# Kernel optimization log

Hardware: AMD Instinct MI355X
Metric: run time of the kernel (lower is better)

## Reference

```python
import jax, jax.numpy as jnp
import numpy as np

B, S, D, H = 4, 2048, 512, 8


def _ln(x, g, b, eps=1e-5):
    m = x.mean(-1, keepdims=True)
    v = ((x - m) ** 2).mean(-1, keepdims=True)
    return (x - m) / jnp.sqrt(v + eps) * g + b


def setup_inputs() -> dict:
    key = jax.random.key(0)
    ks = iter(jax.random.split(key, 32))
    n = lambda shape, s=0.02: jax.random.normal(next(ks), shape, jnp.float32) * s
    z = lambda *shape: jnp.zeros(shape, jnp.float32)
    o = lambda *shape: jnp.ones(shape, jnp.float32)
    return {
        "x": jax.random.normal(next(ks), (B, S, D), jnp.float32),
        "x_prev": jax.random.normal(next(ks), (B, S, D), jnp.float32),
        "mu": jnp.float32(0.5),
        "in_proj_w": n((3 * D, D)), "in_proj_b": z(3 * D),
        "out_w": n((D, D)), "out_b": z(D),
        "ln1_g": o(D), "ln1_b": z(D),
        "time_mod": jnp.full((D,), 0.5, jnp.float32),
        "sm_ln_g": o(D), "sm_ln_b": z(D),
        "wr_w": n((D, D)), "wr_b": z(D),
        "wv_w": n((D, D)), "wv_b": z(D),
        "sc_ln_g": o(D), "sc_ln_b": z(D),
        "ln2_g": o(D), "ln2_b": z(D),
        "w1": n((4 * D, D)), "b1": z(4 * D),
        "w2": n((D, 4 * D)), "b2": z(D),
        "ln3_g": o(D), "ln3_b": z(D),
    }


def reference(x, x_prev, mu, in_proj_w, in_proj_b, out_w, out_b, ln1_g, ln1_b,
              time_mod, sm_ln_g, sm_ln_b, wr_w, wr_b, wv_w, wv_b,
              sc_ln_g, sc_ln_b, ln2_g, ln2_b, w1, b1, w2, b2, ln3_g, ln3_b):
    Bs, Sl, Dm = x.shape
    hd = Dm // H
    # Shift (x_prev is not None)
    shifted = mu * x + (1.0 - mu) * x_prev
    # Multihead self-attention (eval mode; dropout = identity)
    qkv = shifted @ in_proj_w.T + in_proj_b
    q, k, v = jnp.split(qkv, 3, axis=-1)
    q = q.reshape(Bs, Sl, H, hd)
    k = k.reshape(Bs, Sl, H, hd)
    v = v.reshape(Bs, Sl, H, hd)
    scores = jnp.einsum('bqhd,bkhd->bhqk', q, k) / jnp.sqrt(jnp.float32(hd))
    attn = jax.nn.softmax(scores, axis=-1)
    ao = jnp.einsum('bhqk,bkhd->bqhd', attn, v).reshape(Bs, Sl, Dm)
    ao = ao @ out_w.T + out_b
    x1 = _ln(shifted + ao, ln1_g, ln1_b)
    # SequenceMergingSeq with C = V = W = x1: sequential decayed running sums
    def step(carry, xt):  # xt: [B, D]
        a, b = carry
        decay = jax.nn.sigmoid(xt * time_mod)
        e = jnp.exp(xt)
        a = decay.mean(-1, keepdims=True) * a + e.sum(-1, keepdims=True)
        b = decay * b + e * xt
        return (a, b), b / (a + 1e-8)
    a0 = jnp.zeros((Bs, 1), x1.dtype)
    b0 = jnp.zeros((Bs, Dm), x1.dtype)
    _, outs = jax.lax.scan(step, (a0, b0), jnp.swapaxes(x1, 0, 1))  # [S,B,D]
    merged = _ln(jnp.swapaxes(outs, 0, 1), sm_ln_g, sm_ln_b)
    # StateCoupling
    coupled = _ln(jax.nn.sigmoid(merged @ wr_w.T + wr_b) * (merged @ wv_w.T + wv_b),
                  sc_ln_g, sc_ln_b)
    x2 = _ln(x1 + coupled, ln2_g, ln2_b)
    # FFN
    ffn = jax.nn.relu(x2 @ w1.T + b1) @ w2.T + b2
    return _ln(x2 + ffn, ln3_g, ln3_b)
```

## Files before the change

kernel.cpp:

```cpp
#include <hip/hip_runtime.h>
#include <math.h>

#define D_MODEL 512
#define SEQ     2048
#define BATCH   4
#define NH      8
#define HD      64
#define CHUNK   32
#define NCHUNK  64
#define M_TOK   (BATCH*SEQ)

typedef __attribute__((ext_vector_type(8))) short bhalf8;
typedef __attribute__((ext_vector_type(4))) float f32x4;

__device__ __forceinline__ float sigmoidf_(float x){ return 1.f/(1.f+expf(-x)); }

__device__ __forceinline__ unsigned short f2b(float f){
  unsigned u = __float_as_uint(f);
  u += 0x7FFFu + ((u>>16)&1u);
  return (unsigned short)(u>>16);
}
__device__ __forceinline__ float b2f(unsigned short h){
  return __uint_as_float(((unsigned)h)<<16);
}
__device__ __forceinline__ float blo(unsigned v){ return __uint_as_float(v<<16); }
__device__ __forceinline__ float bhi(unsigned v){ return __uint_as_float(v & 0xFFFF0000u); }
__device__ __forceinline__ unsigned bpack(float a, float b){
  return (unsigned)f2b(a) | ((unsigned)f2b(b)<<16);
}

__device__ __forceinline__ void gll16(const void* g, void* l){
  __builtin_amdgcn_global_load_lds(
      (const __attribute__((address_space(1))) unsigned int*)g,
      (__attribute__((address_space(3))) unsigned int*)l, 16, 0, 0);
}

__device__ __forceinline__ float exp2_hw(float x){
  float r;
  asm volatile("v_exp_f32 %0, %1" : "=v"(r) : "v"(x));
  return r;
}

__device__ __forceinline__ void block_sum2(float& a, float& b, float* lds){
  #pragma unroll
  for (int o=32;o>0;o>>=1){ a += __shfl_xor(a,o); b += __shfl_xor(b,o); }
  int w = threadIdx.x>>6, l = threadIdx.x&63;
  if (l==0){ lds[2*w]=a; lds[2*w+1]=b; }
  __syncthreads();
  float ta=0.f, tb=0.f; int nw = blockDim.x>>6;
  for (int i=0;i<nw;++i){ ta+=lds[2*i]; tb+=lds[2*i+1]; }
  a=ta; b=tb;
  __syncthreads();
}

__global__ void cvtshift_k(const float* __restrict__ s0,const float* __restrict__ s1,
                           const float* __restrict__ s2,const float* __restrict__ s3,
                           const float* __restrict__ s4,const float* __restrict__ s5,
                           unsigned short* __restrict__ d0,unsigned short* __restrict__ d1,
                           unsigned short* __restrict__ d2,unsigned short* __restrict__ d3,
                           unsigned short* __restrict__ d4,unsigned short* __restrict__ d5,
                           const float* __restrict__ x, const float* __restrict__ xp,
                           const float* __restrict__ mu,
                           unsigned short* __restrict__ ob){
  int t = blockIdx.x*blockDim.x + threadIdx.x;
  if (t < 917504){
    int j = t;
    const float* s; unsigned short* d;
    if (j < 196608){ s=s0; d=d0; }
    else if ((j-=196608) < 65536){ s=s1; d=d1; }
    else if ((j-=65536)  < 65536){ s=s2; d=d2; }
    else if ((j-=65536)  < 65536){ s=s3; d=d3; }
    else if ((j-=65536)  < 262144){ s=s4; d=d4; }
    else { j-=262144; s=s5; d=d5; }
    float4 v = ((const float4*)s)[j];
    uint2 p; p.x = bpack(v.x, v.y); p.y = bpack(v.z, v.w);
    ((uint2*)d)[j] = p;
  } else {
    int i = t - 917504;
    float m = mu[0];
    float4 a = ((const float4*)x)[i], p = ((const float4*)xp)[i];
    float4 r;
    r.x = m*a.x + (1.f-m)*p.x; r.y = m*a.y + (1.f-m)*p.y;
    r.z = m*a.z + (1.f-m)*p.z; r.w = m*a.w + (1.f-m)*p.w;
    uint2 q; q.x = bpack(r.x, r.y); q.y = bpack(r.z, r.w);
    ((uint2*)ob)[i] = q;
  }
}

template<int ACT, int OUTB>
__global__ __launch_bounds__(256) void mgemm_k(const unsigned short* __restrict__ A,
    const unsigned short* __restrict__ W, const float* __restrict__ bias,
    float* __restrict__ Yf, unsigned short* __restrict__ Yb, int Nd, int K){
  __shared__ unsigned short As[128*64];
  __shared__ unsigned short Bs[128*64];
  const int tid = threadIdx.x;
  const int w = tid>>6, lane = tid&63;
  const int l15 = lane&15, l4 = lane>>4;
  const int wr = w>>1, wc = w&1;
  const int nwg = gridDim.x*gridDim.y;
  const int orig = blockIdx.y*gridDim.x + blockIdx.x;
  const int swz = (orig&7)*(nwg>>3) + (orig>>3);
  const int bn = swz % gridDim.x;
  const int bm = swz / gridDim.x;

  const size_t Kb = (size_t)K*2;
  const int srow  = lane>>3;
  const int sbyte = ((lane&7)*16) ^ (srow<<4);
  const char* Ag = (const char*)A + (size_t)(bm*128)*Kb + sbyte;
  const char* Wg = (const char*)W + (size_t)(bn*128)*Kb + sbyte;

  f32x4 acc[4][4];
  const f32x4 z = {0.f,0.f,0.f,0.f};
  #pragma unroll
  for (int i=0;i<4;++i)
    #pragma unroll
    for (int j=0;j<4;++j) acc[i][j] = z;

  const int KT = K/64;
  for (int kt=0; kt<KT; ++kt){
    if (kt) __syncthreads();
    const size_t kOff = (size_t)kt*128;
    #pragma unroll
    for (int i=0;i<4;++i){
      int c = w*4 + i;
      int r = c*8 + srow;
      gll16(Ag + (size_t)r*Kb + kOff, (char*)As + c*1024);
      gll16(Wg + (size_t)r*Kb + kOff, (char*)Bs + c*1024);
    }
    __syncthreads();

    bhalf8 af[4][2], bf_[4][2];
    #pragma unroll
    for (int fr=0; fr<4; ++fr){
      int row = wr*64 + fr*16 + l15;
      #pragma unroll
      for (int ks=0; ks<2; ++ks){
        int byo = (l4*16 + ks*64) ^ ((row&7)<<4);
        af[fr][ks] = *(const bhalf8*)((const char*)As + row*128 + byo);
      }
    }
    #pragma unroll
    for (int fc=0; fc<4; ++fc){
      int row = wc*64 + fc*16 + l15;
      #pragma unroll
      for (int ks=0; ks<2; ++ks){
        int byo = (l4*16 + ks*64) ^ ((row&7)<<4);
        bf_[fc][ks] = *(const bhalf8*)((const char*)Bs + row*128 + byo);
      }
    }
    #pragma unroll
    for (int ks=0; ks<2; ++ks)
      #pragma unroll
      for (int fr=0; fr<4; ++fr)
        #pragma unroll
        for (int fc=0; fc<4; ++fc)
          acc[fr][fc] = __builtin_amdgcn_mfma_f32_16x16x32_bf16(af[fr][ks], bf_[fc][ks], acc[fr][fc], 0, 0, 0);
  }

  const int rowBase = bm*128 + wr*64;
  const int colBase = bn*128 + wc*64;
  #pragma unroll
  for (int fc=0; fc<4; ++fc){
    int col = colBase + fc*16 + l15;
    float bv = bias[col];
    #pragma unroll
    for (int fr=0; fr<4; ++fr){
      #pragma unroll
      for (int j=0; j<4; ++j){
        int row = rowBase + fr*16 + l4*4 + j;
        float v = acc[fr][fc][j] + bv;
        if (ACT) v = fmaxf(v, 0.f);
        if (OUTB) Yb[(size_t)row*Nd + col] = f2b(v);
        else      Yf[(size_t)row*Nd + col] = v;
      }
    }
  }
}

template<int ACT, int FUSE2, int SPLITK>
__global__ __launch_bounds__(256) void mgemm64_k(const unsigned short* __restrict__ A,
    const unsigned short* __restrict__ W0, const unsigned short* __restrict__ W1v,
    const float* __restrict__ bias0, const float* __restrict__ bias1,
    unsigned short* __restrict__ Yb0, unsigned short* __restrict__ Yb1,
    int Nd, int K){
  __shared__ unsigned short As[128*64];
  __shared__ unsigned short Bs[64*64];
  const int tid = threadIdx.x;
  const int w = tid>>6, lane = tid&63;
  const int l15 = lane&15, l4 = lane>>4;
  const int wr = w>>1, wc = w&1;
  const int nwg = gridDim.x*gridDim.y;
  const int orig = blockIdx.y*gridDim.x + blockIdx.x;
  const int swz = (orig&7)*(nwg>>3) + (orig>>3);
  int bn = swz % gridDim.x;
  const int bm = swz / gridDim.x;
  const unsigned short* W = W0;
  const float* bias = bias0;
  unsigned short* Yb = Yb0;
  int half = 0;
  if (FUSE2 && bn >= 8){ W = W1v; bias = bias1; Yb = Yb1; bn -= 8; }
  if (SPLITK && bn >= 8){ half = 1; Yb = Yb1; bn -= 8; }

  const int Ksr = SPLITK ? (K>>1) : K;
  const size_t Kb = (size_t)K*2;
  const size_t hOff = (size_t)half * Ksr * 2;
  const int srow  = lane>>3;
  const int sbyte = ((lane&7)*16) ^ (srow<<4);
  const char* Ag = (const char*)A + (size_t)(bm*128)*Kb + hOff + sbyte;
  const char* Wg = (const char*)W + (size_t)(bn*64)*Kb + hOff + sbyte;

  f32x4 acc[4][2];
  const f32x4 z = {0.f,0.f,0.f,0.f};
  #pragma unroll
  for (int i=0;i<4;++i)
    #pragma unroll
    for (int j=0;j<2;++j) acc[i][j] = z;

  const int KT = Ksr/64;
  for (int kt=0; kt<KT; ++kt){
    if (kt) __syncthreads();
    const size_t kOff = (size_t)kt*128;
    #pragma unroll
    for (int i=0;i<4;++i){
      int c = w*4 + i;
      int r = c*8 + srow;
      gll16(Ag + (size_t)r*Kb + kOff, (char*)As + c*1024);
    }
    #pragma unroll
    for (int i=0;i<2;++i){
      int c = w*2 + i;
      int r = c*8 + srow;
      gll16(Wg + (size_t)r*Kb + kOff, (char*)Bs + c*1024);
    }
    __syncthreads();

    bhalf8 af[4][2], bf_[2][2];
    #pragma unroll
    for (int fr=0; fr<4; ++fr){
      int row = wr*64 + fr*16 + l15;
      #pragma unroll
      for (int ks=0; ks<2; ++ks){
        int byo = (l4*16 + ks*64) ^ ((row&7)<<4);
        af[fr][ks] = *(const bhalf8*)((const char*)As + row*128 + byo);
      }
    }
    #pragma unroll
    for (int fc=0; fc<2; ++fc){
      int row = wc*32 + fc*16 + l15;
      #pragma unroll
      for (int ks=0; ks<2; ++ks){
        int byo = (l4*16 + ks*64) ^ ((row&7)<<4);
        bf_[fc][ks] = *(const bhalf8*)((const char*)Bs + row*128 + byo);
      }
    }
    #pragma unroll
    for (int ks=0; ks<2; ++ks)
      #pragma unroll
      for (int fr=0; fr<4; ++fr)
        #pragma unroll
        for (int fc=0; fc<2; ++fc)
          acc[fr][fc] = __builtin_amdgcn_mfma_f32_16x16x32_bf16(af[fr][ks], bf_[fc][ks], acc[fr][fc], 0, 0, 0);
  }

  const int rowBase = bm*128 + wr*64;
  const int colBase = bn*64 + wc*32;
  #pragma unroll
  for (int fc=0; fc<2; ++fc){
    int col = colBase + fc*16 + l15;
    float bv = (SPLITK && half) ? 0.f : bias[col];
    #pragma unroll
    for (int fr=0; fr<4; ++fr){
      #pragma unroll
      for (int j=0; j<4; ++j){
        int row = rowBase + fr*16 + l4*4 + j;
        float v = acc[fr][fc][j] + bv;
        if (ACT) v = fmaxf(v, 0.f);
        Yb[(size_t)row*Nd + col] = f2b(v);
      }
    }
  }
}

__global__ __launch_bounds__(512, 4) void fattn_k(const unsigned short* __restrict__ qkv,
                                                  unsigned short* __restrict__ ao){
  __shared__ unsigned short Ks[2][64*64];
  __shared__ unsigned short Vt[2][64*64];
  __shared__ unsigned short Ps[128*64];
  const int nwg = gridDim.x*gridDim.y*gridDim.z;
  const int orig = (blockIdx.z*gridDim.y + blockIdx.y)*gridDim.x + blockIdx.x;
  const int swz = (orig&7)*(nwg>>3) + (orig>>3);
  const int qt = swz % gridDim.x;
  const int rem = swz / gridDim.x;
  const int h = rem % gridDim.y;
  const int b = rem / gridDim.y;
  const int tid = threadIdx.x, w = tid>>6, lane = tid&63;
  const int l15 = lane&15, l4 = lane>>4;
  const size_t rowB = 3072;
  const char* base = (const char*)qkv + (size_t)b*SEQ*rowB;
  const char* Kg = base + 1024 + h*128;
  const char* Vg = base + 2048 + h*128;
  const float C2 = 0.18033688f;

  bhalf8 qf[2];
  {
    const char* qrow = base + (size_t)(qt*128 + w*16 + l15)*rowB + h*128;
    qf[0] = *(const bhalf8*)(qrow + l4*16);
    qf[1] = *(const bhalf8*)(qrow + l4*16 + 64);
  }
  bhalf8 v1;
  {
    short o = (l15==0) ? (short)0x3F80 : (short)0;
    v1 = (bhalf8){o,o,o,o,o,o,o,o};
  }

  const f32x4 z = {0.f,0.f,0.f,0.f};
  f32x4 oa[4], ol = z;
  #pragma unroll
  for (int i=0;i<4;++i) oa[i] = z;
  float mj = -INFINITY;

  const int srow  = lane>>3;
  const int sbyte = ((lane&7)*16) ^ (srow<<4);
  const int vd = lane;
  const int vsel = (vd>>3)&1;

  unsigned short vload[8];
  {
    int r = w*8 + srow;
    gll16(Kg + (size_t)r*rowB + sbyte, (char*)Ks[0] + w*1024);
  }
  #pragma unroll
  for (int i=0;i<8;++i)
    vload[i] = *(const unsigned short*)(Vg + (size_t)(w*8 + i)*rowB + vd*2);

  int cur = 0;
  for (int kt=0; kt<SEQ/64; ++kt){
    #pragma unroll
    for (int i=0;i<2;++i){
      int p = i ^ vsel;
      unsigned lo = (unsigned)vload[p*4+0] | ((unsigned)vload[p*4+1]<<16);
      unsigned hi = (unsigned)vload[p*4+2] | ((unsigned)vload[p*4+3]<<16);
      uint2 pk; pk.x = lo; pk.y = hi;
      int byo = (w*16 + p*8) ^ ((vd&7)<<4);
      *(uint2*)((char*)Vt[cur] + vd*128 + byo) = pk;
    }
    __syncthreads();

    if (kt+1 < SEQ/64){
      int r = w*8 + srow;
      gll16(Kg + (size_t)((kt+1)*64 + r)*rowB + sbyte, (char*)Ks[cur^1] + w*1024);
      #pragma unroll
      for (int i=0;i<8;++i)
        vload[i] = *(const unsigned short*)(Vg + (size_t)((kt+1)*64 + w*8 + i)*rowB + vd*2);
    }

    bhalf8 kf[4][2];
    #pragma unroll
    for (int fc=0; fc<4; ++fc){
      int kr = fc*16 + l15;
      #pragma unroll
      for (int ks=0; ks<2; ++ks){
        int byo = (l4*16 + ks*64) ^ ((kr&7)<<4);
        kf[fc][ks] = *(const bhalf8*)((const char*)Ks[cur] + kr*128 + byo);
      }
    }
    f32x4 s[4];
    #pragma unroll
    for (int i=0;i<4;++i) s[i] = z;
    __builtin_amdgcn_s_setprio(1);
    #pragma unroll
    for (int ks=0; ks<2; ++ks)
      #pragma unroll
      for (int fc=0; fc<4; ++fc)
        s[fc] = __builtin_amdgcn_mfma_f32_16x16x32_bf16(kf[fc][ks], qf[ks], s[fc], 0, 0, 0);
    __builtin_amdgcn_s_setprio(0);

    {
      float rm0 = fmaxf(fmaxf(s[0][0],s[0][1]), fmaxf(s[0][2],s[0][3]));
      float rm1 = fmaxf(fmaxf(s[1][0],s[1][1]), fmaxf(s[1][2],s[1][3]));
      float rm2 = fmaxf(fmaxf(s[2][0],s[2][1]), fmaxf(s[2][2],s[2][3]));
      float rm3 = fmaxf(fmaxf(s[3][0],s[3][1]), fmaxf(s[3][2],s[3][3]));
      float rm = fmaxf(fmaxf(rm0,rm1), fmaxf(rm2,rm3));
      rm = fmaxf(rm, __shfl_xor(rm,16));
      rm = fmaxf(rm, __shfl_xor(rm,32));
      float tmax = rm * C2;
      if (__any(tmax > mj + 8.f)){
        float mn = fmaxf(mj, tmax);
        float sc = exp2_hw(mj - mn);
        mj = mn;
        float scj0 = __shfl(sc, l4*4+0), scj1 = __shfl(sc, l4*4+1);
        float scj2 = __shfl(sc, l4*4+2), scj3 = __shfl(sc, l4*4+3);
        #pragma unroll
        for (int fc=0; fc<4; ++fc){
          oa[fc][0] *= scj0; oa[fc][1] *= scj1;
          oa[fc][2] *= scj2; oa[fc][3] *= scj3;
        }
        ol[0] *= scj0; ol[1] *= scj1; ol[2] *= scj2; ol[3] *= scj3;
      }
      int qrow = w*16 + l15;
      #pragma unroll
      for (int fc=0; fc<4; ++fc){
        float p0 = exp2_hw(fmaf(C2, s[fc][0], -mj));
        float p1 = exp2_hw(fmaf(C2, s[fc][1], -mj));
        float p2 = exp2_hw(fmaf(C2, s[fc][2], -mj));
        float p3 = exp2_hw(fmaf(C2, s[fc][3], -mj));
        unsigned lo, hi;
        asm volatile("v_cvt_pk_bf16_f32 %0, %1, %2" : "=v"(lo) : "v"(p0), "v"(p1));
        asm volatile("v_cvt_pk_bf16_f32 %0, %1, %2" : "=v"(hi) : "v"(p2), "v"(p3));
        uint2 pk; pk.x = lo; pk.y = hi;
        int byo = (fc*32 + l4*8) ^ ((l15&7)<<4);
        *(uint2*)((char*)Ps + qrow*128 + byo) = pk;
      }
    }

    bhalf8 vf[4][2];
    #pragma unroll
    for (int fc=0; fc<4; ++fc){
      int d = fc*16 + l15;
      #pragma unroll
      for (int ks=0; ks<2; ++ks){
        int byo = (ks*64 + l4*16) ^ ((d&7)<<4);
        vf[fc][ks] = *(const bhalf8*)((const char*)Vt[cur] + d*128 + byo);
      }
    }
    {
      int qrow = w*16 + l15;
      bhalf8 pf[2];
      #pragma unroll
      for (int ks=0; ks<2; ++ks){
        int byo = (ks*64 + l4*16) ^ ((l15&7)<<4);
        pf[ks] = *(const bhalf8*)((const char*)Ps + qrow*128 + byo);
      }
      __builtin_amdgcn_s_setprio(1);
      #pragma unroll
      for (int ks=0; ks<2; ++ks){
        #pragma unroll
        for (int fc=0; fc<4; ++fc)
          oa[fc] = __builtin_amdgcn_mfma_f32_16x16x32_bf16(pf[ks], vf[fc][ks], oa[fc], 0, 0, 0);
        ol = __builtin_amdgcn_mfma_f32_16x16x32_bf16(pf[ks], v1, ol, 0, 0, 0);
      }
      __builtin_amdgcn_s_setprio(0);
    }
    cur ^= 1;
  }

  {
    float li[4];
    #pragma unroll
    for (int j=0;j<4;++j) li[j] = 1.f/__shfl(ol[j], l4<<4);
    #pragma unroll
    for (int fc=0; fc<4; ++fc){
      int col = h*64 + fc*16 + l15;
      size_t r0 = (size_t)(b*SEQ + qt*128 + w*16 + l4*4);
      ao[(r0+0)*D_MODEL + col] = f2b(oa[fc][0]*li[0]);
      ao[(r0+1)*D_MODEL + col] = f2b(oa[fc][1]*li[1]);
      ao[(r0+2)*D_MODEL + col] = f2b(oa[fc][2]*li[2]);
      ao[(r0+3)*D_MODEL + col] = f2b(oa[fc][3]*li[3]);
    }
  }
}

__global__ __launch_bounds__(256) void lnfin_k(const unsigned int* __restrict__ X2b,
    const unsigned int* __restrict__ F0, const unsigned int* __restrict__ F1,
    const float* __restrict__ g, const float* __restrict__ be, float* __restrict__ outf){
  __shared__ float lds[16];
  const size_t off2 = (size_t)blockIdx.x * 256;
  const int tid = threadIdx.x;
  unsigned xv = X2b[off2+tid], f0 = F0[off2+tid], f1 = F1[off2+tid];
  float a0 = blo(xv) + blo(f0) + blo(f1);
  float a1 = bhi(xv) + bhi(f0) + bhi(f1);
  float s1 = a0+a1, s2 = a0*a0+a1*a1;
  block_sum2(s1, s2, lds);
  float mean = s1 * (1.f/512.f);
  float var  = s2 * (1.f/512.f) - mean*mean;
  float rstd = rsqrtf(var + 1e-5f);
  float2 gg = ((const float2*)g)[tid], bb = ((const float2*)be)[tid];
  float2 r;
  r.x = (a0-mean)*rstd*gg.x + bb.x;
  r.y = (a1-mean)*rstd*gg.y + bb.y;
  ((float2*)outf)[off2+tid] = r;
}

__global__ __launch_bounds__(256) void ln_scan_k(const unsigned int* __restrict__ Ab,
    const unsigned int* __restrict__ Pb,
    const float* __restrict__ g, const float* __restrict__ be, const float* __restrict__ tm,
    unsigned int* __restrict__ x1b, unsigned int* __restrict__ dec, unsigned int* __restrict__ u,
    float* __restrict__ dm, float* __restrict__ es){
  __shared__ float lds[16];
  const size_t row = blockIdx.x;
  const size_t off2 = row * 256;
  const int tid = threadIdx.x;
  unsigned av = Ab[off2+tid], pv = Pb[off2+tid];
  float a0 = blo(av) + blo(pv);
  float a1 = bhi(av) + bhi(pv);
  float s1 = a0+a1, s2 = a0*a0+a1*a1;
  block_sum2(s1, s2, lds);
  float mean = s1 * (1.f/512.f);
  float var  = s2 * (1.f/512.f) - mean*mean;
  float rstd = rsqrtf(var + 1e-5f);
  float2 gg = ((const float2*)g)[tid], bb = ((const float2*)be)[tid], tt = ((const float2*)tm)[tid];
  float r0 = (a0-mean)*rstd*gg.x + bb.x;
  float r1 = (a1-mean)*rstd*gg.y + bb.y;
  x1b[off2+tid] = bpack(r0, r1);
  float dc0 = sigmoidf_(r0*tt.x), dc1 = sigmoidf_(r1*tt.y);
  float e0 = expf(r0), e1 = expf(r1);
  dec[off2+tid] = bpack(dc0, dc1);
  u[off2+tid]   = bpack(e0*r0, e1*r1);
  float dsum = dc0+dc1, esum = e0+e1;
  block_sum2(dsum, esum, lds);
  if (tid==0){ dm[row]=dsum*(1.f/512.f); es[row]=esum; }
}

__global__ __launch_bounds__(256) void ln2x_k(const unsigned int* __restrict__ R,
    const unsigned int* __restrict__ V, const unsigned int* __restrict__ X1,
    const float* __restrict__ g1, const float* __restrict__ b1_,
    const float* __restrict__ g2, const float* __restrict__ b2_,
    unsigned int* __restrict__ x2b){
  __shared__ float lds[16];
  const size_t off2 = (size_t)blockIdx.x * 256;
  const int tid = threadIdx.x;
  unsigned rv = R[off2+tid], vv = V[off2+tid];
  float a0 = sigmoidf_(blo(rv))*blo(vv);
  float a1 = sigmoidf_(bhi(rv))*bhi(vv);
  float s1 = a0+a1, s2 = a0*a0+a1*a1;
  block_sum2(s1, s2, lds);
  float mean = s1*(1.f/512.f);
  float var  = s2*(1.f/512.f) - mean*mean;
  float rstd = rsqrtf(var + 1e-5f);
  float2 g1v = ((const float2*)g1)[tid], b1v = ((const float2*)b1_)[tid];
  float c0 = (a0-mean)*rstd*g1v.x + b1v.x;
  float c1 = (a1-mean)*rstd*g1v.y + b1v.y;
  unsigned x1v = X1[off2+tid];
  float t0 = blo(x1v) + c0, t1 = bhi(x1v) + c1;
  float u1 = t0+t1, u2 = t0*t0+t1*t1;
  block_sum2(u1, u2, lds);
  float mean2 = u1*(1.f/512.f);
  float var2  = u2*(1.f/512.f) - mean2*mean2;
  float rstd2 = rsqrtf(var2 + 1e-5f);
  float2 g2v = ((const float2*)g2)[tid], b2v = ((const float2*)b2_)[tid];
  float r0 = (t0-mean2)*rstd2*g2v.x + b2v.x;
  float r1 = (t1-mean2)*rstd2*g2v.y + b2v.y;
  x2b[off2+tid] = bpack(r0, r1);
}

__global__ __launch_bounds__(256) void bscan_p1(const unsigned int* __restrict__ decay,
    const unsigned int* __restrict__ u, float* __restrict__ Gc, float* __restrict__ Uc){
  const int c = blockIdx.x, b = blockIdx.y, t = threadIdx.x;
  size_t base2 = ((size_t)b*SEQ + (size_t)c*CHUNK)*256 + t;
  float G0=1.f, G1=1.f, U0=0.f, U1=0.f;
  for (int i=0;i<CHUNK;++i){
    unsigned dv = decay[base2 + (size_t)i*256];
    unsigned uv = u[base2 + (size_t)i*256];
    float g0 = blo(dv), g1 = bhi(dv);
    U0 = g0*U0 + blo(uv); G0 *= g0;
    U1 = g1*U1 + bhi(uv); G1 *= g1;
  }
  size_t idx2 = ((size_t)b*NCHUNK + c)*256 + t;
  float2 gv; gv.x=G0; gv.y=G1;
  float2 uv2; uv2.x=U0; uv2.y=U1;
  ((float2*)Gc)[idx2] = gv;
  ((float2*)Uc)[idx2] = uv2;
}

__global__ __launch_bounds__(512) void scan2_k(const float* __restrict__ Gc, const float* __restrict__ Uc,
    float* __restrict__ binit, const float* __restrict__ dm, const float* __restrict__ es,
    float* __restrict__ a_out){
  __shared__ float sG[512], sU[512];
  if (blockIdx.x < 4){
    const int b = blockIdx.x, d = threadIdx.x;
    float cur = 0.f;
    for (int c=0;c<NCHUNK;++c){
      size_t idx = ((size_t)b*NCHUNK + c)*D_MODEL + d;
      binit[idx] = cur;
      cur = Gc[idx]*cur + Uc[idx];
    }
  } else {
    const int b = blockIdx.x - 4, tid = threadIdx.x;
    const float* dmb = dm + (size_t)b*SEQ;
    const float* esb = es + (size_t)b*SEQ;
    const int t0 = tid*4;
    float gi[4], ui[4];
    #pragma unroll
    for (int i=0;i<4;++i){ gi[i]=dmb[t0+i]; ui[i]=esb[t0+i]; }
    float G=1.f, U=0.f;
    #pragma unroll
    for (int i=0;i<4;++i){ U = gi[i]*U + ui[i]; G *= gi[i]; }
    sG[tid]=G; sU[tid]=U;
    __syncthreads();
    for (int off=1; off<512; off<<=1){
      float pg=1.f, pu=0.f;
      bool act = tid >= off;
      if (act){ pg = sG[tid-off]; pu = sU[tid-off]; }
      __syncthreads();
      if (act){ sU[tid] = sG[tid]*pu + sU[tid]; sG[tid] = sG[tid]*pg; }
      __syncthreads();
    }
    float a = (tid==0) ? 0.f : sU[tid-1];
    #pragma unroll
    for (int i=0;i<4;++i){ a = gi[i]*a + ui[i]; a_out[(size_t)b*SEQ + t0 + i] = a; }
  }
}

__global__ __launch_bounds__(256) void p3ln_k(const unsigned int* __restrict__ decay,
    const unsigned int* __restrict__ u,
    const float* __restrict__ binit, const float* __restrict__ a,
    const float* __restrict__ g, const float* __restrict__ be,
    unsigned int* __restrict__ mb){
  __shared__ float lds[16];
  const int c = blockIdx.x, b = blockIdx.y, t = threadIdx.x;
  size_t base2 = ((size_t)b*SEQ + (size_t)c*CHUNK)*256 + t;
  float2 bv = ((const float2*)binit)[((size_t)b*NCHUNK + c)*256 + t];
  float2 gg = ((const float2*)g)[t], bb = ((const float2*)be)[t];
  for (int i=0;i<CHUNK;++i){
    unsigned dv = decay[base2 + (size_t)i*256];
    unsigned uv = u[base2 + (size_t)i*256];
    bv.x = blo(dv)*bv.x + blo(uv);
    bv.y = bhi(dv)*bv.y + bhi(uv);
    float av = a[(size_t)b*SEQ + (size_t)c*CHUNK + i];
    float inv = 1.f/(av + 1e-8f);
    float v0 = bv.x*inv, v1 = bv.y*inv;
    float s1 = v0+v1, s2 = v0*v0+v1*v1;
    block_sum2(s1, s2, lds);
    float mean = s1*(1.f/512.f);
    float var  = s2*(1.f/512.f) - mean*mean;
    float rstd = rsqrtf(var + 1e-5f);
    mb[base2 + (size_t)i*256] = bpack((v0-mean)*rstd*gg.x + bb.x,
                                      (v1-mean)*rstd*gg.y + bb.y);
  }
}

extern "C" void kernel_launch(void* const* d_in, const int* in_sizes, int n_in,
                              void* d_out, int out_size, void* d_ws, size_t ws_size,
                              hipStream_t stream){
  const float* x     = (const float*)d_in[0];
  const float* xp    = (const float*)d_in[1];
  const float* mu    = (const float*)d_in[2];
  const float* in_w  = (const float*)d_in[3];
  const float* in_b  = (const float*)d_in[4];
  const float* out_w = (const float*)d_in[5];
  const float* out_b = (const float*)d_in[6];
  const float* ln1_g = (const float*)d_in[7];
  const float* ln1_b = (const float*)d_in[8];
  const float* tm    = (const float*)d_in[9];
  const float* sm_g  = (const float*)d_in[10];
  const float* sm_b  = (const float*)d_in[11];
  const float* wr_w  = (const float*)d_in[12];
  const float* wr_b  = (const float*)d_in[13];
  const float* wv_w  = (const float*)d_in[14];
  const float* wv_b  = (const float*)d_in[15];
  const float* sc_g  = (const float*)d_in[16];
  const float* sc_b  = (const float*)d_in[17];
  const float* ln2_g = (const float*)d_in[18];
  const float* ln2_b = (const float*)d_in[19];
  const float* w1    = (const float*)d_in[20];
  const float* b1    = (const float*)d_in[21];
  const float* w2    = (const float*)d_in[22];
  const float* b2    = (const float*)d_in[23];
  const float* ln3_g = (const float*)d_in[24];
  const float* ln3_b = (const float*)d_in[25];
  float* out = (float*)d_out;
  float* ws  = (float*)d_ws;

  const size_t N = (size_t)M_TOK*D_MODEL;
  unsigned short* Pb  = (unsigned short*)ws;
  unsigned short* X1b = (unsigned short*)ws + N;
  unsigned short* F0  = (unsigned short*)(ws + N);
  unsigned short* F1  = (unsigned short*)(ws + N) + N;
  float* EX  = ws + 3*N;
  float* dm    = EX;
  float* es    = EX + 8192;
  float* aarr  = EX + 16384;
  float* Gc    = EX + 24576;
  float* Uc    = Gc + 131072;
  float* binit = Uc + 131072;

  unsigned short* SB = (unsigned short*)(ws + 3*N + N/4);
  unsigned short* Wq = SB;
  unsigned short* Wo = Wq + 786432;
  unsigned short* Wr = Wo + 262144;
  unsigned short* Wv = Wr + 262144;
  unsigned short* W1 = Wv + 262144;
  unsigned short* W2 = W1 + 1048576;
  unsigned short* Xb = W2 + 1048576;
  unsigned short* Mb = Xb + N;
  unsigned short* U  = Mb + N;
  unsigned short* Qb  = U;
  unsigned short* AOb = U + 12*1024*1024;
  unsigned short* ub   = U;
  unsigned short* decb = U + 12*1024*1024;
  unsigned short* Rb   = U;
  unsigned short* Vb   = U + 4*1024*1024;
  unsigned short* Hb   = U;

  cvtshift_k<<<7680, 256, 0, stream>>>(in_w, out_w, wr_w, wv_w, w1, w2,
                                       Wq, Wo, Wr, Wv, W1, W2,
                                       x, xp, mu, Xb);
  mgemm_k<0,1><<<dim3(12,64), 256, 0, stream>>>(Xb, Wq, in_b, nullptr, Qb, 1536, 512);
  fattn_k<<<dim3(SEQ/128, NH, BATCH), 512, 0, stream>>>(Qb, AOb);
  mgemm64_k<0,0,0><<<dim3(8,64), 256, 0, stream>>>(AOb, Wo, nullptr, out_b, nullptr,
                                                   Pb, nullptr, 512, 512);
  ln_scan_k<<<M_TOK, 256, 0, stream>>>((const unsigned int*)Xb, (const unsigned int*)Pb,
                                       ln1_g, ln1_b, tm,
                                       (unsigned int*)X1b, (unsigned int*)decb, (unsigned int*)ub,
                                       dm, es);
  bscan_p1<<<dim3(NCHUNK, BATCH), 256, 0, stream>>>((const unsigned int*)decb, (const unsigned int*)ub, Gc, Uc);
  scan2_k<<<8, 512, 0, stream>>>(Gc, Uc, binit, dm, es, aarr);
  p3ln_k<<<dim3(NCHUNK, BATCH), 256, 0, stream>>>((const unsigned int*)decb, (const unsigned int*)ub,
                                                  binit, aarr, sm_g, sm_b, (unsigned int*)Mb);
  mgemm64_k<0,1,0><<<dim3(16,64), 256, 0, stream>>>(Mb, Wr, Wv, wr_b, wv_b,
                                                    Rb, Vb, 512, 512);
  ln2x_k<<<M_TOK, 256, 0, stream>>>((const unsigned int*)Rb, (const unsigned int*)Vb,
                                    (const unsigned int*)X1b,
                                    sc_g, sc_b, ln2_g, ln2_b, (unsigned int*)Xb);
  mgemm_k<1,1><<<dim3(16,64), 256, 0, stream>>>(Xb, W1, b1, nullptr, Hb, 2048, 512);
  mgemm64_k<0,0,1><<<dim3(16,64), 256, 0, stream>>>(Hb, W2, nullptr, b2, nullptr,
                                                    F0, F1, 512, 2048);
  lnfin_k<<<M_TOK, 256, 0, stream>>>((const unsigned int*)Xb, (const unsigned int*)F0,
                                     (const unsigned int*)F1, ln3_g, ln3_b, out);
}
```

Measured before the change: 252.3 us.

## Process two 16-row query tiles per wave in flash attention

```diff
diff --git a/kernel.cpp b/kernel.cpp
--- a/kernel.cpp
+++ b/kernel.cpp
@@ -281,11 +281,11 @@
   }
 }
 
-__global__ __launch_bounds__(512, 4) void fattn_k(const unsigned short* __restrict__ qkv,
+__global__ __launch_bounds__(512, 2) void fattn_k(const unsigned short* __restrict__ qkv,
                                                   unsigned short* __restrict__ ao){
   __shared__ unsigned short Ks[2][64*64];
   __shared__ unsigned short Vt[2][64*64];
-  __shared__ unsigned short Ps[128*64];
+  __shared__ unsigned short Ps[256*64];
   const int nwg = gridDim.x*gridDim.y*gridDim.z;
   const int orig = (blockIdx.z*gridDim.y + blockIdx.y)*gridDim.x + blockIdx.x;
   const int swz = (orig&7)*(nwg>>3) + (orig>>3);
@@ -301,11 +301,12 @@
   const char* Vg = base + 2048 + h*128;
   const float C2 = 0.18033688f;
 
-  bhalf8 qf[2];
-  {
-    const char* qrow = base + (size_t)(qt*128 + w*16 + l15)*rowB + h*128;
-    qf[0] = *(const bhalf8*)(qrow + l4*16);
-    qf[1] = *(const bhalf8*)(qrow + l4*16 + 64);
+  bhalf8 qf[2][2];
+  #pragma unroll
+  for (int t=0;t<2;++t){
+    const char* qrow = base + (size_t)(qt*256 + w*32 + t*16 + l15)*rowB + h*128;
+    qf[t][0] = *(const bhalf8*)(qrow + l4*16);
+    qf[t][1] = *(const bhalf8*)(qrow + l4*16 + 64);
   }
   bhalf8 v1;
   {
@@ -314,10 +315,14 @@
   }
 
   const f32x4 z = {0.f,0.f,0.f,0.f};
-  f32x4 oa[4], ol = z;
-  #pragma unroll
-  for (int i=0;i<4;++i) oa[i] = z;
-  float mj = -INFINITY;
+  f32x4 oa[2][4], ol[2];
+  #pragma unroll
+  for (int t=0;t<2;++t){
+    #pragma unroll
+    for (int i=0;i<4;++i) oa[t][i] = z;
+    ol[t] = z;
+  }
+  float mj[2] = {-INFINITY, -INFINITY};
 
   const int srow  = lane>>3;
   const int sbyte = ((lane&7)*16) ^ (srow<<4);
@@ -364,18 +369,20 @@
         kf[fc][ks] = *(const bhalf8*)((const char*)Ks[cur] + kr*128 + byo);
       }
     }
-    f32x4 s[4];
-    #pragma unroll
-    for (int i=0;i<4;++i) s[i] = z;
-    __builtin_amdgcn_s_setprio(1);
-    #pragma unroll
-    for (int ks=0; ks<2; ++ks)
-      #pragma unroll
-      for (int fc=0; fc<4; ++fc)
-        s[fc] = __builtin_amdgcn_mfma_f32_16x16x32_bf16(kf[fc][ks], qf[ks], s[fc], 0, 0, 0);
-    __builtin_amdgcn_s_setprio(0);
-
-    {
+
+    #pragma unroll
+    for (int t=0; t<2; ++t){
+      f32x4 s[4];
+      #pragma unroll
+      for (int i=0;i<4;++i) s[i] = z;
+      __builtin_amdgcn_s_setprio(1);
+      #pragma unroll
+      for (int ks=0; ks<2; ++ks)
+        #pragma unroll
+        for (int fc=0; fc<4; ++fc)
+          s[fc] = __builtin_amdgcn_mfma_f32_16x16x32_bf16(kf[fc][ks], qf[t][ks], s[fc], 0, 0, 0);
+      __builtin_amdgcn_s_setprio(0);
+
       float rm0 = fmaxf(fmaxf(s[0][0],s[0][1]), fmaxf(s[0][2],s[0][3]));
       float rm1 = fmaxf(fmaxf(s[1][0],s[1][1]), fmaxf(s[1][2],s[1][3]));
       float rm2 = fmaxf(fmaxf(s[2][0],s[2][1]), fmaxf(s[2][2],s[2][3]));
@@ -384,26 +391,26 @@
       rm = fmaxf(rm, __shfl_xor(rm,16));
       rm = fmaxf(rm, __shfl_xor(rm,32));
       float tmax = rm * C2;
-      if (__any(tmax > mj + 8.f)){
-        float mn = fmaxf(mj, tmax);
-        float sc = exp2_hw(mj - mn);
-        mj = mn;
+      if (__any(tmax > mj[t] + 8.f)){
+        float mn = fmaxf(mj[t], tmax);
+        float sc = exp2_hw(mj[t] - mn);
+        mj[t] = mn;
         float scj0 = __shfl(sc, l4*4+0), scj1 = __shfl(sc, l4*4+1);
         float scj2 = __shfl(sc, l4*4+2), scj3 = __shfl(sc, l4*4+3);
         #pragma unroll
         for (int fc=0; fc<4; ++fc){
-          oa[fc][0] *= scj0; oa[fc][1] *= scj1;
-          oa[fc][2] *= scj2; oa[fc][3] *= scj3;
+          oa[t][fc][0] *= scj0; oa[t][fc][1] *= scj1;
+          oa[t][fc][2] *= scj2; oa[t][fc][3] *= scj3;
         }
-        ol[0] *= scj0; ol[1] *= scj1; ol[2] *= scj2; ol[3] *= scj3;
-      }
-      int qrow = w*16 + l15;
+        ol[t][0] *= scj0; ol[t][1] *= scj1; ol[t][2] *= scj2; ol[t][3] *= scj3;
+      }
+      int qrow = w*32 + t*16 + l15;
       #pragma unroll
       for (int fc=0; fc<4; ++fc){
-        float p0 = exp2_hw(fmaf(C2, s[fc][0], -mj));
-        float p1 = exp2_hw(fmaf(C2, s[fc][1], -mj));
-        float p2 = exp2_hw(fmaf(C2, s[fc][2], -mj));
-        float p3 = exp2_hw(fmaf(C2, s[fc][3], -mj));
+        float p0 = exp2_hw(fmaf(C2, s[fc][0], -mj[t]));
+        float p1 = exp2_hw(fmaf(C2, s[fc][1], -mj[t]));
+        float p2 = exp2_hw(fmaf(C2, s[fc][2], -mj[t]));
+        float p3 = exp2_hw(fmaf(C2, s[fc][3], -mj[t]));
         unsigned lo, hi;
         asm volatile("v_cvt_pk_bf16_f32 %0, %1, %2" : "=v"(lo) : "v"(p0), "v"(p1));
         asm volatile("v_cvt_pk_bf16_f32 %0, %1, %2" : "=v"(hi) : "v"(p2), "v"(p3));
@@ -423,8 +430,9 @@
         vf[fc][ks] = *(const bhalf8*)((const char*)Vt[cur] + d*128 + byo);
       }
     }
-    {
-      int qrow = w*16 + l15;
+    #pragma unroll
+    for (int t=0; t<2; ++t){
+      int qrow = w*32 + t*16 + l15;
       bhalf8 pf[2];
       #pragma unroll
       for (int ks=0; ks<2; ++ks){
@@ -436,26 +444,27 @@
       for (int ks=0; ks<2; ++ks){
         #pragma unroll
         for (int fc=0; fc<4; ++fc)
-          oa[fc] = __builtin_amdgcn_mfma_f32_16x16x32_bf16(pf[ks], vf[fc][ks], oa[fc], 0, 0, 0);
-        ol = __builtin_amdgcn_mfma_f32_16x16x32_bf16(pf[ks], v1, ol, 0, 0, 0);
+          oa[t][fc] = __builtin_amdgcn_mfma_f32_16x16x32_bf16(pf[ks], vf[fc][ks], oa[t][fc], 0, 0, 0);
+        ol[t] = __builtin_amdgcn_mfma_f32_16x16x32_bf16(pf[ks], v1, ol[t], 0, 0, 0);
       }
       __builtin_amdgcn_s_setprio(0);
     }
     cur ^= 1;
   }
 
-  {
+  #pragma unroll
+  for (int t=0; t<2; ++t){
     float li[4];
     #pragma unroll
-    for (int j=0;j<4;++j) li[j] = 1.f/__shfl(ol[j], l4<<4);
+    for (int j=0;j<4;++j) li[j] = 1.f/__shfl(ol[t][j], l4<<4);
     #pragma unroll
     for (int fc=0; fc<4; ++fc){
       int col = h*64 + fc*16 + l15;
-      size_t r0 = (size_t)(b*SEQ + qt*128 + w*16 + l4*4);
-      ao[(r0+0)*D_MODEL + col] = f2b(oa[fc][0]*li[0]);
-      ao[(r0+1)*D_MODEL + col] = f2b(oa[fc][1]*li[1]);
-      ao[(r0+2)*D_MODEL + col] = f2b(oa[fc][2]*li[2]);
-      ao[(r0+3)*D_MODEL + col] = f2b(oa[fc][3]*li[3]);
+      size_t r0 = (size_t)(b*SEQ + qt*256 + w*32 + t*16 + l4*4);
+      ao[(r0+0)*D_MODEL + col] = f2b(oa[t][fc][0]*li[0]);
+      ao[(r0+1)*D_MODEL + col] = f2b(oa[t][fc][1]*li[1]);
+      ao[(r0+2)*D_MODEL + col] = f2b(oa[t][fc][2]*li[2]);
+      ao[(r0+3)*D_MODEL + col] = f2b(oa[t][fc][3]*li[3]);
     }
   }
 }
@@ -696,7 +705,7 @@
                                        Wq, Wo, Wr, Wv, W1, W2,
                                        x, xp, mu, Xb);
   mgemm_k<0,1><<<dim3(12,64), 256, 0, stream>>>(Xb, Wq, in_b, nullptr, Qb, 1536, 512);
-  fattn_k<<<dim3(SEQ/128, NH, BATCH), 512, 0, stream>>>(Qb, AOb);
+  fattn_k<<<dim3(SEQ/256, NH, BATCH), 512, 0, stream>>>(Qb, AOb);
   mgemm64_k<0,0,0><<<dim3(8,64), 256, 0, stream>>>(AOb, Wo, nullptr, out_b, nullptr,
                                                    Pb, nullptr, 512, 512);
   ln_scan_k<<<M_TOK, 256, 0, stream>>>((const unsigned int*)Xb, (const unsigned int*)Pb,
```

Result: slower. 262.7 us (+4.1%).
